# Performance work log

Measured on AMD Instinct MI355X. Metric: run time of the kernel, lower is better.

The kernel has to match this reference:

```python
import jax, jax.numpy as jnp
import numpy as np
from jax import lax

EPS = 1e-8  # pix_norm epsilon (PGGAN convention)


def _conv2d_valid(x, w, b):
    # x: [B,H,W,Cin], w: [kh,kw,Cin,Cout] -> relu(conv) valid padding
    y = lax.conv_general_dilated(x, w, window_strides=(1, 1), padding='VALID',
                                 dimension_numbers=('NHWC', 'HWIO', 'NHWC'))
    return jax.nn.relu(y + b)


def _parametric_depthwise(x, filters):
    # x: [B,H,W,C], filters: [B,kh,kw,C] -> per-sample depthwise conv, SAME, stride 1
    C = x.shape[-1]

    def one(xb, fb):
        # xb: [H,W,C], fb: [kh,kw,C]; depthwise kernel HWIO with I=1, groups=C
        y = lax.conv_general_dilated(xb[None], fb[:, :, None, :], window_strides=(1, 1),
                                     padding='SAME',
                                     dimension_numbers=('NHWC', 'HWIO', 'NHWC'),
                                     feature_group_count=C)
        return y[0]

    return jax.vmap(one)(x, filters)


def setup_inputs() -> dict:
    key = jax.random.key(0)
    ks = jax.random.split(key, 10)
    B, H, W, C = 16, 512, 512, 4
    P, E, F = 8, 128, 4
    s = lambda k, shape, fan: jax.random.normal(k, shape, jnp.float32) * (1.0 / np.sqrt(fan))
    return {
        'input_noise': jax.random.normal(ks[0], (B, H, W, C), jnp.float32),
        'input_params': jax.random.normal(ks[1], (B, P), jnp.float32),
        'W_emb': s(ks[2], (P, E), P),          # Dense(128)
        'b_emb': jnp.zeros((E,), jnp.float32),
        'KT': s(ks[3], (3, 3, E, F), E),        # Conv2DTranspose kernel (acts on 1x1 input)
        'bT': jnp.zeros((F,), jnp.float32),
        'W1': s(ks[4], (9, 9, C, F), 9 * 9 * C),  # gen-init-conv
        'b1': jnp.zeros((F,), jnp.float32),
        'W2': s(ks[5], (9, 9, F, F), 9 * 9 * F),  # gen-init-conv2
        'b2': jnp.zeros((F,), jnp.float32),
    }


def reference(input_noise, input_params, W_emb, b_emb, KT, bT, W1, b1, W2, b2):
    # Dense(128, swish)
    emb = jax.nn.silu(input_params @ W_emb + b_emb)  # [B,128]
    # Reshape to [B,1,1,128] + Conv2DTranspose(k=3, s=3, same): each output pixel (i,j)
    # of the 3x3 grid is input * KT[i,j]; swish activation.
    filters = jax.nn.silu(jnp.einsum('bc,ijcf->bijf', emb, KT) + bT)  # [B,3,3,4]
    # Conv2D(4, 9x9, valid, relu)
    y = _conv2d_valid(input_noise, W1, b1)  # [B,H-8,W-8,4]
    # per-sample dynamic depthwise conv (SAME)
    y = _parametric_depthwise(y, filters)
    # Conv2D(4, 9x9, valid, relu)
    y = _conv2d_valid(y, W2, b2)  # [B,H-16,W-16,4]
    # pix_norm: channelwise RMS normalization
    y = y * lax.rsqrt(jnp.mean(jnp.square(y), axis=-1, keepdims=True) + EPS)
    return y
```

## Files before the change

### kernel.cpp

```cpp
#include <hip/hip_runtime.h>


typedef _Float16 f16;
typedef _Float16 f16x2 __attribute__((ext_vector_type(2)));
typedef _Float16 f16x4 __attribute__((ext_vector_type(4)));
typedef _Float16 f16x8 __attribute__((ext_vector_type(8)));
typedef float f32x4 __attribute__((ext_vector_type(4)));

static __device__ __forceinline__ f32x4 mfma16(f16x8 a, f16x8 b, f32x4 c) {
    return __builtin_amdgcn_mfma_f32_16x16x32_f16(a, b, c, 0, 0, 0);
}

static __device__ __forceinline__ float silu_f(float x) {
    return x / (1.0f + expf(-x));
}

static __device__ __forceinline__ f16x2 split_f(float x) {
    f16x2 r;
    r[0] = (f16)x;
    r[1] = (f16)(x - (float)r[0]);
    return r;
}

template <int D0, int ND, int NR, bool PRIO>
static __device__ __forceinline__ void conv_chunk(
    const f16x8* __restrict__ bbase, const f16x4 (*__restrict__ s_hi)[76],
    const f16x4 (*__restrict__ s_lo)[76], const int wrow, const int aoff,
    f32x4* __restrict__ acc)
{
    f16x8 Bh[ND], Bl[ND];
#pragma unroll
    for (int j = 0; j < ND; ++j) {
        Bh[j] = bbase[(D0 + j) * 256];
        Bl[j] = bbase[(D0 + j) * 256 + 64];
    }
    if (PRIO) __builtin_amdgcn_s_setprio(1);
#pragma unroll
    for (int ir = D0; ir < D0 + ND + NR - 1; ++ir) {
        const f16x8 Ah = *(const f16x8*)(&s_hi[wrow + ir][0] + aoff);
        const f16x8 Al = *(const f16x8*)(&s_lo[wrow + ir][0] + aoff);
#pragma unroll
        for (int r = 0; r < NR; ++r) {
            const int dy = ir - r;
            if (dy >= D0 && dy < D0 + ND) {
                acc[r] = mfma16(Ah, Bh[dy - D0], acc[r]);
                acc[r] = mfma16(Ah, Bl[dy - D0], acc[r]);
                acc[r] = mfma16(Al, Bh[dy - D0], acc[r]);
            }
        }
    }
    if (PRIO) __builtin_amdgcn_s_setprio(0);
}

__global__ __launch_bounds__(256) void k_prep(
    const float* __restrict__ params, const float* __restrict__ W_emb,
    const float* __restrict__ b_emb, const float* __restrict__ KT,
    const float* __restrict__ bT, const float* __restrict__ W1,
    const float* __restrict__ W2,
    f16x8* __restrict__ fragW1, f16x8* __restrict__ fragW2)
{
    __shared__ float s_emb[128];
    __shared__ float s_filt[36];
    __shared__ float s_wc[1936];
    const int t = threadIdx.x, b = blockIdx.x;

    if (t < 128) {
        float sv = b_emb[t];
#pragma unroll
        for (int p = 0; p < 8; ++p)
            sv = fmaf(params[b * 8 + p], W_emb[p * 128 + t], sv);
        s_emb[t] = silu_f(sv);
    }
    __syncthreads();
    if (t < 36) {
        const int ij = t >> 2, ff = t & 3;
        float sv = bT[ff];
        for (int c = 0; c < 128; ++c)
            sv = fmaf(s_emb[c], KT[(ij * 128 + c) * 4 + ff], sv);
        s_filt[t] = silu_f(sv);
    }
    __syncthreads();

    for (int i = t; i < 1936; i += 256) {
        const int f = i & 3, c = (i >> 2) & 3;
        const int dxy = i >> 4, dx = dxy % 11, dy = dxy / 11;
        float sv = 0.f;
#pragma unroll
        for (int i2 = 0; i2 < 3; ++i2)
#pragma unroll
            for (int j2 = 0; j2 < 3; ++j2) {
                const int a = dy - i2, bb = dx - j2;
                if (a >= 0 && a < 9 && bb >= 0 && bb < 9)
                    sv = fmaf(s_filt[(i2 * 3 + j2) * 4 + c],
                              W2[((a * 9 + bb) * 4 + c) * 4 + f], sv);
            }
        s_wc[i] = sv;
    }
    __syncthreads();

    for (int fi = t; fi < 11 * 256; fi += 256) {
        const int dy = fi >> 8, rem = fi & 255;
        const int st = (rem >> 7) & 1, hl = (rem >> 6) & 1, lane = rem & 63;
        const int g = lane >> 4, n = lane & 15, s = n >> 2, f = n & 3;
        f16x8 v;
#pragma unroll
        for (int j = 0; j < 8; ++j) {
            const int k = st * 32 + g * 8 + j;
            const int e = k >> 2, c = k & 3, dx = e - s;
            const float wv = (dx >= 0 && dx < 11)
                ? s_wc[((dy * 11 + dx) * 4 + c) * 4 + f] : 0.f;
            const f16x2 hlv = split_f(wv);
            v[j] = hl ? hlv[1] : hlv[0];
        }
        fragW2[((size_t)b * 11 + dy) * 256 + rem] = v;
    }

    if (b == 0) {
        for (int fi = t; fi < 9 * 256; fi += 256) {
            const int dy = fi >> 8, rem = fi & 255;
            const int st = (rem >> 7) & 1, hl = (rem >> 6) & 1, lane = rem & 63;
            const int g = lane >> 4, n = lane & 15, s = n >> 2, f = n & 3;
            f16x8 v;
#pragma unroll
            for (int j = 0; j < 8; ++j) {
                const int k = st * 32 + g * 8 + j;
                const int e = k >> 2, c = k & 3, dx = e - s;
                const float wv = (dx >= 0 && dx < 9)
                    ? W1[((dy * 9 + dx) * 4 + c) * 4 + f] : 0.f;
                const f16x2 hlv = split_f(wv);
                v[j] = hl ? hlv[1] : hlv[0];
            }
            fragW1[(size_t)dy * 256 + rem] = v;
        }
    }
}

__global__ __launch_bounds__(256, 2) void k_conv1(
    const float* __restrict__ in, const float* __restrict__ b1,
    const f16x8* __restrict__ fragW1, f16* __restrict__ y1)
{
    __shared__ f16x4 s_hi[40][76];
    __shared__ f16x4 s_lo[40][76];
    const int t = threadIdx.x;
    const int x0 = blockIdx.x * 64, y0 = blockIdx.y * 32, b = blockIdx.z;

    const float4* inp = (const float4*)in + (size_t)b * (512 * 512);
    for (int i = t; i < 40 * 76; i += 256) {
        const int rr = i / 76, cc = i % 76;
        const int gy = y0 + rr, gx = x0 + cc;
        float4 v = make_float4(0.f, 0.f, 0.f, 0.f);
        if (gy < 512 && gx < 512) v = inp[gy * 512 + gx];
        f16x4 h, l;
        const f16x2 p0 = split_f(v.x), p1 = split_f(v.y);
        const f16x2 p2 = split_f(v.z), p3 = split_f(v.w);
        h[0] = p0[0]; l[0] = p0[1]; h[1] = p1[0]; l[1] = p1[1];
        h[2] = p2[0]; l[2] = p2[1]; h[3] = p3[0]; l[3] = p3[1];
        s_hi[rr][cc] = h; s_lo[rr][cc] = l;
    }

    const int lane = t & 63, w = t >> 6;
    const int g = lane >> 4, n = lane & 15, s = n >> 2, f = n & 3;

    __syncthreads();

    const float bias = b1[f];
    f32x4 acc[8];
#pragma unroll
    for (int r = 0; r < 8; ++r) acc[r] = (f32x4){bias, bias, bias, bias};

    const int ai = 4 * (lane & 15) + 2 * g;
#pragma unroll
    for (int st = 0; st < 2; ++st) {
        const f16x8* bbase = fragW1 + st * 128 + lane;
        const int aoff = ai + st * 8;
        conv_chunk<0, 5, 8, false>(bbase, s_hi, s_lo, w * 8, aoff, acc);
        conv_chunk<5, 4, 8, false>(bbase, s_hi, s_lo, w * 8, aoff, acc);
    }

    const int xb = x0 + 16 * g + s;
#pragma unroll
    for (int r = 0; r < 8; ++r) {
        const int yr = y0 + w * 8 + r;
        if (yr >= 504) continue;
        const size_t rowbase = ((size_t)(b * 504 + yr) * 504) * 8 + f * 2;
#pragma unroll
        for (int q = 0; q < 4; ++q) {
            const int x = xb + 4 * q;
            if (x < 504) {
                const float v = fmaxf(acc[r][q], 0.f);
                *(f16x2*)(y1 + rowbase + (size_t)x * 8) = split_f(v);
            }
        }
    }
}

__global__ __launch_bounds__(256, 2) void k_dwconv2(
    const f16* __restrict__ y1, const float* __restrict__ b2,
    const f16x8* __restrict__ fragW2, float* __restrict__ out)
{
    __shared__ f16x4 s_hi[26][76];
    __shared__ f16x4 s_lo[26][76];
    const int t = threadIdx.x;
    const int x0 = blockIdx.x * 64, y0 = blockIdx.y * 16, b = blockIdx.z;

    for (int i = t; i < 26 * 76; i += 256) {
        const int rr = i / 76, cc = i % 76;
        const int gy = y0 - 1 + rr, gx = x0 - 1 + cc;
        f16x4 h, l;
        if (gy >= 0 && gy < 504 && gx >= 0 && gx < 504) {
            const f16x8 p = *(const f16x8*)(y1 + ((size_t)(b * 504 + gy) * 504 +
                                                  (size_t)gx) * 8);
            h[0] = p[0]; l[0] = p[1]; h[1] = p[2]; l[1] = p[3];
            h[2] = p[4]; l[2] = p[5]; h[3] = p[6]; l[3] = p[7];
        } else {
            h[0] = h[1] = h[2] = h[3] = (f16)0.f;
            l[0] = l[1] = l[2] = l[3] = (f16)0.f;
        }
        s_hi[rr][cc] = h; s_lo[rr][cc] = l;
    }

    const int lane = t & 63, w = t >> 6;
    const int g = lane >> 4, n = lane & 15, s = n >> 2, f = n & 3;
    const f16x8* fr = fragW2 + (size_t)b * 11 * 256;

    __syncthreads();

    const float bias = b2[f];
    f32x4 acc[4];
#pragma unroll
    for (int r = 0; r < 4; ++r) acc[r] = (f32x4){bias, bias, bias, bias};

    const int ai = 4 * (lane & 15) + 2 * g;
#pragma unroll
    for (int st = 0; st < 2; ++st) {
        const f16x8* bbase = fr + st * 128 + lane;
        const int aoff = ai + st * 8;
        conv_chunk<0, 4, 4, true>(bbase, s_hi, s_lo, w * 4, aoff, acc);
        conv_chunk<4, 4, 4, true>(bbase, s_hi, s_lo, w * 4, aoff, acc);
        conv_chunk<8, 3, 4, true>(bbase, s_hi, s_lo, w * 4, aoff, acc);
    }

    const int xb = x0 + 16 * g + s;
#pragma unroll
    for (int r = 0; r < 4; ++r) {
        const int yr = y0 + w * 4 + r;
        const size_t rowbase = ((size_t)((size_t)b * 496 + yr) * 496) * 4 + f;
#pragma unroll
        for (int q = 0; q < 4; ++q) {
            float v = fmaxf(acc[r][q], 0.f);
            float sq = v * v;
            sq += __shfl_xor(sq, 1);
            sq += __shfl_xor(sq, 2);
            const float sc = rsqrtf(sq * 0.25f + 1e-8f);
            const int x = xb + 4 * q;
            if (yr < 496 && x < 496) out[rowbase + (size_t)x * 4] = v * sc;
        }
    }
}

extern "C" void kernel_launch(void* const* d_in, const int* in_sizes, int n_in,
                              void* d_out, int out_size, void* d_ws, size_t ws_size,
                              hipStream_t stream)
{
    const float* noise  = (const float*)d_in[0];
    const float* params = (const float*)d_in[1];
    const float* W_emb  = (const float*)d_in[2];
    const float* b_emb  = (const float*)d_in[3];
    const float* KT     = (const float*)d_in[4];
    const float* bT     = (const float*)d_in[5];
    const float* W1     = (const float*)d_in[6];
    const float* b1     = (const float*)d_in[7];
    const float* W2     = (const float*)d_in[8];
    const float* b2     = (const float*)d_in[9];

    float* out = (float*)d_out;
    f16*   y1  = (f16*)d_ws;
    f16x8* fragW2 = (f16x8*)((char*)d_ws + 65028096);
    f16x8* fragW1 = (f16x8*)((char*)d_ws + 65028096 + 720896);

    k_prep<<<dim3(16), dim3(256), 0, stream>>>(params, W_emb, b_emb, KT, bT,
                                               W1, W2, fragW1, fragW2);

    dim3 grid(8, 16, 16);
    k_conv1<<<grid, dim3(256), 0, stream>>>(noise, b1, fragW1, y1);

    dim3 grid2(8, 31, 16);
    k_dwconv2<<<grid2, dim3(256), 0, stream>>>(y1, b2, fragW2, out);
}
```

Before: 130.3 us.

## Split intermediate into hi/lo planes and read conv2 operands directly from global

After: 160.1 us. 1.23x slower.

```diff
diff --git a/kernel.cpp b/kernel.cpp
--- a/kernel.cpp
+++ b/kernel.cpp
@@ -22,7 +22,12 @@
     return r;
 }
 
-template <int D0, int ND, int NR, bool PRIO>
+static __device__ __forceinline__ void zero_half(f16x8& v, int h) {
+    if (h == 0) { v[0] = (f16)0.f; v[1] = (f16)0.f; v[2] = (f16)0.f; v[3] = (f16)0.f; }
+    else        { v[4] = (f16)0.f; v[5] = (f16)0.f; v[6] = (f16)0.f; v[7] = (f16)0.f; }
+}
+
+template <int D0, int ND, int NR>
 static __device__ __forceinline__ void conv_chunk(
     const f16x8* __restrict__ bbase, const f16x4 (*__restrict__ s_hi)[76],
     const f16x4 (*__restrict__ s_lo)[76], const int wrow, const int aoff,
@@ -34,7 +39,6 @@
         Bh[j] = bbase[(D0 + j) * 256];
         Bl[j] = bbase[(D0 + j) * 256 + 64];
     }
-    if (PRIO) __builtin_amdgcn_s_setprio(1);
 #pragma unroll
     for (int ir = D0; ir < D0 + ND + NR - 1; ++ir) {
         const f16x8 Ah = *(const f16x8*)(&s_hi[wrow + ir][0] + aoff);
@@ -49,7 +53,51 @@
             }
         }
     }
-    if (PRIO) __builtin_amdgcn_s_setprio(0);
+}
+
+template <int D0, int ND, int NR>
+static __device__ __forceinline__ void conv_chunk_glob(
+    const f16x8* __restrict__ bbase,
+    const f16* __restrict__ y1h, const f16* __restrict__ y1l,
+    const int b, const int y0row, const int gxp, const bool xedge,
+    f32x4* __restrict__ acc)
+{
+    f16x8 Bh[ND], Bl[ND];
+#pragma unroll
+    for (int j = 0; j < ND; ++j) {
+        Bh[j] = bbase[(D0 + j) * 256];
+        Bl[j] = bbase[(D0 + j) * 256 + 64];
+    }
+    __builtin_amdgcn_s_setprio(1);
+#pragma unroll
+    for (int ir = D0; ir < D0 + ND + NR - 1; ++ir) {
+        const int gy = y0row + ir - 1;
+        f16x8 Ah, Al;
+        if (gy < 0 || gy > 503) {
+#pragma unroll
+            for (int j = 0; j < 8; ++j) { Ah[j] = (f16)0.f; Al[j] = (f16)0.f; }
+        } else {
+            const int gc  = gxp;
+            const int gcc = min(max(gc, 0), 502);
+            const size_t off = ((size_t)(b * 504 + gy) * 504 + (size_t)gcc) * 4;
+            Ah = *(const f16x8*)(y1h + off);
+            Al = *(const f16x8*)(y1l + off);
+            if (xedge) {
+                if (gc < 0 || gc > 503) { zero_half(Ah, 0); zero_half(Al, 0); }
+                if (gc + 1 < 0 || gc + 1 > 503) { zero_half(Ah, 1); zero_half(Al, 1); }
+            }
+        }
+#pragma unroll
+        for (int r = 0; r < NR; ++r) {
+            const int dy = ir - r;
+            if (dy >= D0 && dy < D0 + ND) {
+                acc[r] = mfma16(Ah, Bh[dy - D0], acc[r]);
+                acc[r] = mfma16(Ah, Bl[dy - D0], acc[r]);
+                acc[r] = mfma16(Al, Bh[dy - D0], acc[r]);
+            }
+        }
+    }
+    __builtin_amdgcn_s_setprio(0);
 }
 
 __global__ __launch_bounds__(256) void k_prep(
@@ -106,9 +154,9 @@
 #pragma unroll
         for (int j = 0; j < 8; ++j) {
             const int k = st * 32 + g * 8 + j;
-            const int e = k >> 2, c = k & 3, dx = e - s;
-            const float wv = (dx >= 0 && dx < 11)
-                ? s_wc[((dy * 11 + dx) * 4 + c) * 4 + f] : 0.f;
+            const int e = k >> 2, c = k & 3, dxp = e - s;
+            const float wv = (dxp >= 1 && dxp < 12)
+                ? s_wc[((dy * 11 + (dxp - 1)) * 4 + c) * 4 + f] : 0.f;
             const f16x2 hlv = split_f(wv);
             v[j] = hl ? hlv[1] : hlv[0];
         }
@@ -137,7 +185,8 @@
 
 __global__ __launch_bounds__(256, 2) void k_conv1(
     const float* __restrict__ in, const float* __restrict__ b1,
-    const f16x8* __restrict__ fragW1, f16* __restrict__ y1)
+    const f16x8* __restrict__ fragW1,
+    f16* __restrict__ y1h, f16* __restrict__ y1l)
 {
     __shared__ f16x4 s_hi[40][76];
     __shared__ f16x4 s_lo[40][76];
@@ -173,8 +222,8 @@
     for (int st = 0; st < 2; ++st) {
         const f16x8* bbase = fragW1 + st * 128 + lane;
         const int aoff = ai + st * 8;
-        conv_chunk<0, 5, 8, false>(bbase, s_hi, s_lo, w * 8, aoff, acc);
-        conv_chunk<5, 4, 8, false>(bbase, s_hi, s_lo, w * 8, aoff, acc);
+        conv_chunk<0, 5, 8>(bbase, s_hi, s_lo, w * 8, aoff, acc);
+        conv_chunk<5, 4, 8>(bbase, s_hi, s_lo, w * 8, aoff, acc);
     }
 
     const int xb = x0 + 16 * g + s;
@@ -182,48 +231,32 @@
     for (int r = 0; r < 8; ++r) {
         const int yr = y0 + w * 8 + r;
         if (yr >= 504) continue;
-        const size_t rowbase = ((size_t)(b * 504 + yr) * 504) * 8 + f * 2;
+        const size_t rowbase = ((size_t)(b * 504 + yr) * 504) * 4 + f;
 #pragma unroll
         for (int q = 0; q < 4; ++q) {
             const int x = xb + 4 * q;
             if (x < 504) {
                 const float v = fmaxf(acc[r][q], 0.f);
-                *(f16x2*)(y1 + rowbase + (size_t)x * 8) = split_f(v);
-            }
-        }
-    }
-}
-
-__global__ __launch_bounds__(256, 2) void k_dwconv2(
-    const f16* __restrict__ y1, const float* __restrict__ b2,
+                const f16x2 p = split_f(v);
+                y1h[rowbase + (size_t)x * 4] = p[0];
+                y1l[rowbase + (size_t)x * 4] = p[1];
+            }
+        }
+    }
+}
+
+__global__ __launch_bounds__(256) void k_dwconv2(
+    const f16* __restrict__ y1h, const f16* __restrict__ y1l,
+    const float* __restrict__ b2,
     const f16x8* __restrict__ fragW2, float* __restrict__ out)
 {
-    __shared__ f16x4 s_hi[26][76];
-    __shared__ f16x4 s_lo[26][76];
     const int t = threadIdx.x;
     const int x0 = blockIdx.x * 64, y0 = blockIdx.y * 16, b = blockIdx.z;
-
-    for (int i = t; i < 26 * 76; i += 256) {
-        const int rr = i / 76, cc = i % 76;
-        const int gy = y0 - 1 + rr, gx = x0 - 1 + cc;
-        f16x4 h, l;
-        if (gy >= 0 && gy < 504 && gx >= 0 && gx < 504) {
-            const f16x8 p = *(const f16x8*)(y1 + ((size_t)(b * 504 + gy) * 504 +
-                                                  (size_t)gx) * 8);
-            h[0] = p[0]; l[0] = p[1]; h[1] = p[2]; l[1] = p[3];
-            h[2] = p[4]; l[2] = p[5]; h[3] = p[6]; l[3] = p[7];
-        } else {
-            h[0] = h[1] = h[2] = h[3] = (f16)0.f;
-            l[0] = l[1] = l[2] = l[3] = (f16)0.f;
-        }
-        s_hi[rr][cc] = h; s_lo[rr][cc] = l;
-    }
 
     const int lane = t & 63, w = t >> 6;
     const int g = lane >> 4, n = lane & 15, s = n >> 2, f = n & 3;
     const f16x8* fr = fragW2 + (size_t)b * 11 * 256;
-
-    __syncthreads();
+    const bool xedge = (blockIdx.x == 0) || (blockIdx.x == 7);
 
     const float bias = b2[f];
     f32x4 acc[4];
@@ -231,13 +264,14 @@
     for (int r = 0; r < 4; ++r) acc[r] = (f32x4){bias, bias, bias, bias};
 
     const int ai = 4 * (lane & 15) + 2 * g;
+    const int y0row = y0 + w * 4;
 #pragma unroll
     for (int st = 0; st < 2; ++st) {
         const f16x8* bbase = fr + st * 128 + lane;
-        const int aoff = ai + st * 8;
-        conv_chunk<0, 4, 4, true>(bbase, s_hi, s_lo, w * 4, aoff, acc);
-        conv_chunk<4, 4, 4, true>(bbase, s_hi, s_lo, w * 4, aoff, acc);
-        conv_chunk<8, 3, 4, true>(bbase, s_hi, s_lo, w * 4, aoff, acc);
+        const int gxp = x0 - 2 + ai + st * 8;
+        conv_chunk_glob<0, 4, 4>(bbase, y1h, y1l, b, y0row, gxp, xedge, acc);
+        conv_chunk_glob<4, 4, 4>(bbase, y1h, y1l, b, y0row, gxp, xedge, acc);
+        conv_chunk_glob<8, 3, 4>(bbase, y1h, y1l, b, y0row, gxp, xedge, acc);
     }
 
     const int xb = x0 + 16 * g + s;
@@ -274,7 +308,8 @@
     const float* b2     = (const float*)d_in[9];
 
     float* out = (float*)d_out;
-    f16*   y1  = (f16*)d_ws;
+    f16* y1h = (f16*)d_ws;
+    f16* y1l = (f16*)((char*)d_ws + 32514048);
     f16x8* fragW2 = (f16x8*)((char*)d_ws + 65028096);
     f16x8* fragW1 = (f16x8*)((char*)d_ws + 65028096 + 720896);
 
@@ -282,8 +317,8 @@
                                                W1, W2, fragW1, fragW2);
 
     dim3 grid(8, 16, 16);
-    k_conv1<<<grid, dim3(256), 0, stream>>>(noise, b1, fragW1, y1);
+    k_conv1<<<grid, dim3(256), 0, stream>>>(noise, b1, fragW1, y1h, y1l);
 
     dim3 grid2(8, 31, 16);
-    k_dwconv2<<<grid2, dim3(256), 0, stream>>>(y1, b2, fragW2, out);
-}
+    k_dwconv2<<<grid2, dim3(256), 0, stream>>>(y1h, y1l, b2, fragW2, out);
+}
```

## Process two row tiles per block in dwconv2 with register-prefetched second tile

Applied to the files above, without the earlier changes.

Measured after the change: 134.7 us. 3.4% more time.

```diff
diff --git a/kernel.cpp b/kernel.cpp
--- a/kernel.cpp
+++ b/kernel.cpp
@@ -201,59 +201,135 @@
     __shared__ f16x4 s_hi[26][76];
     __shared__ f16x4 s_lo[26][76];
     const int t = threadIdx.x;
-    const int x0 = blockIdx.x * 64, y0 = blockIdx.y * 16, b = blockIdx.z;
-
-    for (int i = t; i < 26 * 76; i += 256) {
-        const int rr = i / 76, cc = i % 76;
-        const int gy = y0 - 1 + rr, gx = x0 - 1 + cc;
-        f16x4 h, l;
-        if (gy >= 0 && gy < 504 && gx >= 0 && gx < 504) {
-            const f16x8 p = *(const f16x8*)(y1 + ((size_t)(b * 504 + gy) * 504 +
-                                                  (size_t)gx) * 8);
-            h[0] = p[0]; l[0] = p[1]; h[1] = p[2]; l[1] = p[3];
-            h[2] = p[4]; l[2] = p[5]; h[3] = p[6]; l[3] = p[7];
-        } else {
-            h[0] = h[1] = h[2] = h[3] = (f16)0.f;
-            l[0] = l[1] = l[2] = l[3] = (f16)0.f;
-        }
-        s_hi[rr][cc] = h; s_lo[rr][cc] = l;
-    }
+    const int x0 = blockIdx.x * 64, y0 = blockIdx.y * 32, b = blockIdx.z;
 
     const int lane = t & 63, w = t >> 6;
     const int g = lane >> 4, n = lane & 15, s = n >> 2, f = n & 3;
     const f16x8* fr = fragW2 + (size_t)b * 11 * 256;
-
-    __syncthreads();
-
     const float bias = b2[f];
-    f32x4 acc[4];
-#pragma unroll
-    for (int r = 0; r < 4; ++r) acc[r] = (f32x4){bias, bias, bias, bias};
-
     const int ai = 4 * (lane & 15) + 2 * g;
-#pragma unroll
-    for (int st = 0; st < 2; ++st) {
-        const f16x8* bbase = fr + st * 128 + lane;
-        const int aoff = ai + st * 8;
-        conv_chunk<0, 4, 4, true>(bbase, s_hi, s_lo, w * 4, aoff, acc);
-        conv_chunk<4, 4, 4, true>(bbase, s_hi, s_lo, w * 4, aoff, acc);
-        conv_chunk<8, 3, 4, true>(bbase, s_hi, s_lo, w * 4, aoff, acc);
-    }
-
     const int xb = x0 + 16 * g + s;
-#pragma unroll
-    for (int r = 0; r < 4; ++r) {
-        const int yr = y0 + w * 4 + r;
-        const size_t rowbase = ((size_t)((size_t)b * 496 + yr) * 496) * 4 + f;
-#pragma unroll
-        for (int q = 0; q < 4; ++q) {
-            float v = fmaxf(acc[r][q], 0.f);
-            float sq = v * v;
-            sq += __shfl_xor(sq, 1);
-            sq += __shfl_xor(sq, 2);
-            const float sc = rsqrtf(sq * 0.25f + 1e-8f);
-            const int x = xb + 4 * q;
-            if (yr < 496 && x < 496) out[rowbase + (size_t)x * 4] = v * sc;
+
+    f16x8 p0a[8];
+#pragma unroll
+    for (int it = 0; it < 8; ++it) {
+        const int i = it * 256 + t;
+        f16x8 p;
+#pragma unroll
+        for (int j = 0; j < 8; ++j) p[j] = (f16)0.f;
+        if (i < 26 * 76) {
+            const int rr = i / 76, cc = i % 76;
+            const int gy = y0 - 1 + rr, gx = x0 - 1 + cc;
+            if (gy >= 0 && gy < 504 && gx >= 0 && gx < 504)
+                p = *(const f16x8*)(y1 + ((size_t)(b * 504 + gy) * 504 +
+                                          (size_t)gx) * 8);
+        }
+        p0a[it] = p;
+    }
+#pragma unroll
+    for (int it = 0; it < 8; ++it) {
+        const int i = it * 256 + t;
+        if (i < 26 * 76) {
+            const f16x8 p = p0a[it];
+            f16x4 h, l;
+            h[0] = p[0]; l[0] = p[1]; h[1] = p[2]; l[1] = p[3];
+            h[2] = p[4]; l[2] = p[5]; h[3] = p[6]; l[3] = p[7];
+            s_hi[i / 76][i % 76] = h; s_lo[i / 76][i % 76] = l;
+        }
+    }
+    __syncthreads();
+
+    const bool haveT1 = (y0 + 16) < 496;
+    f16x8 p1a[8];
+    if (haveT1) {
+#pragma unroll
+        for (int it = 0; it < 8; ++it) {
+            const int i = it * 256 + t;
+            f16x8 p;
+#pragma unroll
+            for (int j = 0; j < 8; ++j) p[j] = (f16)0.f;
+            if (i < 26 * 76) {
+                const int rr = i / 76, cc = i % 76;
+                const int gy = y0 + 15 + rr, gx = x0 - 1 + cc;
+                if (gy >= 0 && gy < 504 && gx >= 0 && gx < 504)
+                    p = *(const f16x8*)(y1 + ((size_t)(b * 504 + gy) * 504 +
+                                              (size_t)gx) * 8);
+            }
+            p1a[it] = p;
+        }
+    }
+
+    {
+        f32x4 acc[4];
+#pragma unroll
+        for (int r = 0; r < 4; ++r) acc[r] = (f32x4){bias, bias, bias, bias};
+#pragma unroll
+        for (int st = 0; st < 2; ++st) {
+            const f16x8* bbase = fr + st * 128 + lane;
+            const int aoff = ai + st * 8;
+            conv_chunk<0, 4, 4, true>(bbase, s_hi, s_lo, w * 4, aoff, acc);
+            conv_chunk<4, 4, 4, true>(bbase, s_hi, s_lo, w * 4, aoff, acc);
+            conv_chunk<8, 3, 4, true>(bbase, s_hi, s_lo, w * 4, aoff, acc);
+        }
+#pragma unroll
+        for (int r = 0; r < 4; ++r) {
+            const int yr = y0 + w * 4 + r;
+            const size_t rowbase = ((size_t)((size_t)b * 496 + yr) * 496) * 4 + f;
+#pragma unroll
+            for (int q = 0; q < 4; ++q) {
+                float v = fmaxf(acc[r][q], 0.f);
+                float sq = v * v;
+                sq += __shfl_xor(sq, 1);
+                sq += __shfl_xor(sq, 2);
+                const float sc = rsqrtf(sq * 0.25f + 1e-8f);
+                const int x = xb + 4 * q;
+                if (yr < 496 && x < 496) out[rowbase + (size_t)x * 4] = v * sc;
+            }
+        }
+    }
+
+    if (!haveT1) return;
+    __syncthreads();
+#pragma unroll
+    for (int it = 0; it < 8; ++it) {
+        const int i = it * 256 + t;
+        if (i < 26 * 76) {
+            const f16x8 p = p1a[it];
+            f16x4 h, l;
+            h[0] = p[0]; l[0] = p[1]; h[1] = p[2]; l[1] = p[3];
+            h[2] = p[4]; l[2] = p[5]; h[3] = p[6]; l[3] = p[7];
+            s_hi[i / 76][i % 76] = h; s_lo[i / 76][i % 76] = l;
+        }
+    }
+    __syncthreads();
+
+    {
+        f32x4 acc[4];
+#pragma unroll
+        for (int r = 0; r < 4; ++r) acc[r] = (f32x4){bias, bias, bias, bias};
+#pragma unroll
+        for (int st = 0; st < 2; ++st) {
+            const f16x8* bbase = fr + st * 128 + lane;
+            const int aoff = ai + st * 8;
+            conv_chunk<0, 4, 4, true>(bbase, s_hi, s_lo, w * 4, aoff, acc);
+            conv_chunk<4, 4, 4, true>(bbase, s_hi, s_lo, w * 4, aoff, acc);
+            conv_chunk<8, 3, 4, true>(bbase, s_hi, s_lo, w * 4, aoff, acc);
+        }
+        const int y1b = y0 + 16;
+#pragma unroll
+        for (int r = 0; r < 4; ++r) {
+            const int yr = y1b + w * 4 + r;
+            const size_t rowbase = ((size_t)((size_t)b * 496 + yr) * 496) * 4 + f;
+#pragma unroll
+            for (int q = 0; q < 4; ++q) {
+                float v = fmaxf(acc[r][q], 0.f);
+                float sq = v * v;
+                sq += __shfl_xor(sq, 1);
+                sq += __shfl_xor(sq, 2);
+                const float sc = rsqrtf(sq * 0.25f + 1e-8f);
+                const int x = xb + 4 * q;
+                if (yr < 496 && x < 496) out[rowbase + (size_t)x * 4] = v * sc;
+            }
         }
     }
 }
@@ -284,6 +360,6 @@
     dim3 grid(8, 16, 16);
     k_conv1<<<grid, dim3(256), 0, stream>>>(noise, b1, fragW1, y1);
 
-    dim3 grid2(8, 31, 16);
+    dim3 grid2(8, 16, 16);
     k_dwconv2<<<grid2, dim3(256), 0, stream>>>(y1, b2, fragW2, out);
 }
```
